# Kernel tuning notes

Hardware: AMD Instinct MI355X
Metric: run time of the kernel (lower is better)

The kernel has to match this reference:

```python
import jax, jax.numpy as jnp
import numpy as np

LEAKY_SLOPE = 0.01  # torch nn.LeakyReLU default

def leaky_relu(x):
    return jnp.where(x >= 0, x, LEAKY_SLOPE * x)

def setup_inputs() -> dict:
    key = jax.random.key(0)
    ks = jax.random.split(key, 11)
    B, F, C_IN, H, K, D = 2048, 512, 3, 64, 8, 128  # batch, features, expand, layer_conf[0], bucket_num, bucket_dim
    ASR, MM, OUT = 128, 768, 256
    proj_in = ASR + MM + F * D
    inp = {
        "stat_features": jax.random.uniform(ks[0], (B, F), dtype=jnp.float32),
        "asr_embeddings": jax.random.normal(ks[1], (B, ASR), dtype=jnp.float32),
        "mm_embeddings": jax.random.normal(ks[2], (B, MM), dtype=jnp.float32),
        "linear1_w": jax.random.normal(ks[3], (F, C_IN, H), dtype=jnp.float32) * (1.0 / np.sqrt(C_IN)),
        "linear1_b": jax.random.normal(ks[4], (F, 1, H), dtype=jnp.float32),
        "linear2_w": jax.random.normal(ks[5], (F, H, K), dtype=jnp.float32) * (1.0 / np.sqrt(H)),
        "linear2_b": jax.random.normal(ks[6], (F, 1, K), dtype=jnp.float32),
        "tau": jnp.ones((F, 1, K), dtype=jnp.float32),
        "emb": jax.random.normal(ks[7], (F, K, D), dtype=jnp.float32),
        "proj_w": jax.random.normal(ks[8], (OUT, proj_in), dtype=jnp.float32) * (1.0 / np.sqrt(proj_in)),
        "proj_b": jax.random.normal(ks[9], (OUT,), dtype=jnp.float32) * 0.01,
    }
    return inp

def reference(stat_features, asr_embeddings, mm_embeddings,
              linear1_w, linear1_b, linear2_w, linear2_b, tau, emb,
              proj_w, proj_b):
    # sanitize: NaN -> 0, negatives -> 0
    x = stat_features
    x = jnp.where(jnp.isnan(x) | (x < 0.0), 0.0, x)  # [B, F]

    # auto_dis: per-feature tiny MLP. x is expanded to 3 identical copies -> [B,F,1,3]
    # matmul with [F,3,H] == einsum over the 3 copies.
    B, F = x.shape
    x3 = jnp.broadcast_to(x[:, :, None], (B, F, 3))           # [B,F,3]
    h = jnp.einsum('bfc,fch->bfh', x3, linear1_w) + linear1_b[:, 0, :]  # [B,F,H]
    h = jnp.where(h >= 0, h, LEAKY_SLOPE * h)
    s = jnp.einsum('bfh,fhk->bfk', h, linear2_w) + linear2_b[:, 0, :]   # [B,F,K]
    s = jnp.where(s >= 0, s, LEAKY_SLOPE * s)
    s = s * tau[:, 0, :]
    p = jax.nn.softmax(s, axis=-1)                            # [B,F,K]
    y = jnp.einsum('bfk,fkd->bfd', p, emb)                    # [B,F,D]
    y = y.reshape(B, -1)                                      # [B, F*D] (fc = Identity)

    z = jnp.concatenate([asr_embeddings, mm_embeddings, y], axis=1)
    out = jax.nn.relu(z @ proj_w.T + proj_b)                  # [B, 256]
    return out
```

## Files before the change

### kernel.cpp

```cpp
#include <hip/hip_runtime.h>
#include <hip/hip_bf16.h>
#include <math.h>

#define LEAKY 0.01f
#define B_    2048
#define F_    512
#define H_    64
#define K_    8
#define D_    128
#define ASR_  128
#define MM_   768
#define OUT_  256
#define PROJ_IN 66432
#define ZK    4992
#define NSPLIT 8


typedef unsigned short u16;
typedef u16   u16x4 __attribute__((ext_vector_type(4)));
typedef u16   u16x8 __attribute__((ext_vector_type(8)));
typedef short s16x8 __attribute__((ext_vector_type(8)));
typedef float f32x4 __attribute__((ext_vector_type(4)));

__device__ __forceinline__ u16 f2bf(float x) {
  unsigned int u = __float_as_uint(x);
  u += 0x7fffu + ((u >> 16) & 1u);
  return (u16)(u >> 16);
}

#define PRODUCER_BLOCKS (2048 + 512 + 896 + 224)

__global__ __launch_bounds__(256) void producer_kernel(
    const float* __restrict__ stat, const float* __restrict__ w1,
    const float* __restrict__ b1v, const float* __restrict__ w2,
    const float* __restrict__ b2v, const float* __restrict__ tauv,
    const float* __restrict__ pw, const float* __restrict__ emb,
    const float* __restrict__ asr, const float* __restrict__ mm,
    u16* __restrict__ A0, u16* __restrict__ Pf, u16* __restrict__ Wn) {
  __shared__ __align__(16) char smem[20992];
  const int bid = blockIdx.x;
  const int t = threadIdx.x;

  if (bid < 2048) {
    const int f = bid >> 2;
    const int o0 = (bid & 3) * 64;
    float* s_emb = (float*)smem;
    for (int i = t; i < K_ * D_; i += 256) s_emb[i] = emb[(size_t)f * K_ * D_ + i];
    __syncthreads();
    const int orow = t >> 2, dc = t & 3;
    const float* src = pw + (size_t)(o0 + orow) * PROJ_IN + 896 + f * D_;
    float g[K_] = {0.f, 0.f, 0.f, 0.f, 0.f, 0.f, 0.f, 0.f};
    #pragma unroll
    for (int j = 0; j < 8; ++j) {
      const int d = dc * 4 + j * 16;
      float4 w = *(const float4*)(src + d);
      #pragma unroll
      for (int k = 0; k < K_; ++k) {
        float4 e = *(const float4*)(s_emb + k * D_ + d);
        g[k] = fmaf(w.x, e.x, g[k]);
        g[k] = fmaf(w.y, e.y, g[k]);
        g[k] = fmaf(w.z, e.z, g[k]);
        g[k] = fmaf(w.w, e.w, g[k]);
      }
    }
    #pragma unroll
    for (int k = 0; k < K_; ++k) {
      g[k] += __shfl_xor(g[k], 1);
      g[k] += __shfl_xor(g[k], 2);
    }
    if (dc == 0) {
      u16x8 hv;
      #pragma unroll
      for (int k = 0; k < K_; ++k) hv[k] = f2bf(g[k]);
      *(u16x8*)(Wn + (size_t)(o0 + orow) * ZK + 896 + f * K_) = hv;
    }
  } else if (bid < 2560) {
    const int pb = bid - 2048;
    const int f0 = (pb & 127) * 4;
    const int b0 = (pb >> 7) * 512;
    float* s_w1s = (float*)(smem);
    float* s_b1  = (float*)(smem + 1024);
    float* s_w2  = (float*)(smem + 2048);
    float* s_b2  = (float*)(smem + 10240);
    float* s_tau = (float*)(smem + 10368);
    float* s_x   = (float*)(smem + 10496);
    {
      int fl = t >> 6, h = t & 63;
      const float* wf = w1 + (size_t)(f0 + fl) * 192;
      s_w1s[fl * 64 + h] = wf[h] + wf[64 + h] + wf[128 + h];
      s_b1[fl * 64 + h] = b1v[(size_t)(f0 + fl) * 64 + h];
    }
    for (int i = t; i < 4 * 512; i += 256) {
      int fl = i >> 9, idx = i & 511;
      s_w2[fl * 512 + idx] = w2[(size_t)(f0 + fl) * 512 + idx];
    }
    if (t < 32) {
      s_b2[t]  = b2v[f0 * 8 + t];
      s_tau[t] = tauv[f0 * 8 + t];
    }
    for (int p = 0; p < 8; ++p) {
      int i = p * 256 + t;
      int r = i >> 2, fl = i & 3;
      float v = stat[(size_t)(b0 + r) * F_ + f0 + fl];
      s_x[r * 5 + fl] = (v >= 0.f) ? v : 0.f;
    }
    __syncthreads();

    const int w = t >> 6;
    const int lane = t & 63;
    const float* w1p = s_w1s + w * 64;
    const float* b1p = s_b1 + w * 64;
    const float* w2p = s_w2 + w * 512;
    float x[8];
    #pragma unroll
    for (int p = 0; p < 8; ++p) x[p] = s_x[(lane + 64 * p) * 5 + w];
    float acc[8][8] = {{0.f}};
    #pragma unroll 4
    for (int i = 0; i < 64; ++i) {
      float wv = w1p[i], bv = b1p[i];
      float4 wa = *(const float4*)(w2p + i * 8);
      float4 wb = *(const float4*)(w2p + i * 8 + 4);
      #pragma unroll
      for (int p = 0; p < 8; ++p) {
        float h0 = fmaf(x[p], wv, bv);
        float h = fmaf(LEAKY, fminf(h0, 0.f), fmaxf(h0, 0.f));
        acc[p][0] = fmaf(h, wa.x, acc[p][0]);
        acc[p][1] = fmaf(h, wa.y, acc[p][1]);
        acc[p][2] = fmaf(h, wa.z, acc[p][2]);
        acc[p][3] = fmaf(h, wa.w, acc[p][3]);
        acc[p][4] = fmaf(h, wb.x, acc[p][4]);
        acc[p][5] = fmaf(h, wb.y, acc[p][5]);
        acc[p][6] = fmaf(h, wb.z, acc[p][6]);
        acc[p][7] = fmaf(h, wb.w, acc[p][7]);
      }
    }
    #pragma unroll
    for (int p = 0; p < 8; ++p) {
      float s[K_];
      float m = -1e30f;
      #pragma unroll
      for (int k = 0; k < K_; ++k) {
        float v = acc[p][k] + s_b2[w * 8 + k];
        v = (v >= 0.f) ? v : LEAKY * v;
        v *= s_tau[w * 8 + k];
        s[k] = v;
        m = fmaxf(m, v);
      }
      float sum = 0.f;
      #pragma unroll
      for (int k = 0; k < K_; ++k) { s[k] = __expf(s[k] - m); sum += s[k]; }
      float inv = 1.f / sum;
      u16x8 hv;
      #pragma unroll
      for (int k = 0; k < K_; ++k) hv[k] = f2bf(s[k] * inv);
      *(u16x8*)(Pf + ((size_t)(f0 + w) * B_ + b0 + lane + 64 * p) * 8) = hv;
    }
  } else if (bid < 3456) {
    const int item = bid - 2560;
    const int cidx = item * 256 + t;
    const int r = cidx / 112, c = cidx % 112;
    float4 v0, v1;
    if (c < 16) {
      const float* s = asr + (size_t)r * ASR_ + c * 8;
      v0 = *(const float4*)(s); v1 = *(const float4*)(s + 4);
    } else {
      const float* s = mm + (size_t)r * MM_ + (c - 16) * 8;
      v0 = *(const float4*)(s); v1 = *(const float4*)(s + 4);
    }
    u16x8 hv = {f2bf(v0.x), f2bf(v0.y), f2bf(v0.z), f2bf(v0.w),
                f2bf(v1.x), f2bf(v1.y), f2bf(v1.z), f2bf(v1.w)};
    *(u16x8*)(A0 + (size_t)r * 896 + c * 8) = hv;
  } else {
    const int item = bid - 3456;
    #pragma unroll
    for (int rr = 0; rr < 4; ++rr) {
      int idx = item * 1024 + rr * 256 + t;
      int o = idx / 896, j = idx % 896;
      Wn[(size_t)o * ZK + j] = f2bf(pw[(size_t)o * PROJ_IN + j]);
    }
  }
}

#define SAS 72
__global__ __launch_bounds__(256) void gemm_kernel(
    const u16* __restrict__ A0, const u16* __restrict__ Pf,
    const u16* __restrict__ Wn, float* __restrict__ part) {
  const int bm0 = blockIdx.x * 64;
  const int bn0 = blockIdx.y * 64;
  const int kz  = blockIdx.z;
  const int it0 = kz * 10;
  const int itn = (kz == 7) ? 8 : 10;
  __shared__ u16 sA[64 * SAS];
  __shared__ u16 sB[64 * SAS];
  const int t = threadIdx.x;
  const int w = t >> 6, L = t & 63;
  const int l16 = L & 15, q8 = (L >> 4) * 8;
  const int wm = (w >> 1) * 32, wn = (w & 1) * 32;
  const int row = t >> 2, lk = t & 3;
  f32x4 acc[2][2] = {{{0.f,0.f,0.f,0.f},{0.f,0.f,0.f,0.f}},
                     {{0.f,0.f,0.f,0.f},{0.f,0.f,0.f,0.f}}};
  u16x8 ra[2], rb[2];

#define LOAD_TILES(IT)                                                        \
  {                                                                           \
    const int k0_ = (IT) * 64;                                                \
    if (k0_ < 896) {                                                          \
      const u16* s_ = A0 + (size_t)(bm0 + row) * 896 + k0_ + lk * 8;          \
      ra[0] = *(const u16x8*)(s_);                                            \
      ra[1] = *(const u16x8*)(s_ + 32);                                       \
    } else {                                                                  \
      const int fb_ = (k0_ - 896) >> 3;                                       \
      ra[0] = *(const u16x8*)(Pf + ((size_t)(fb_ + lk) * B_ + bm0 + row) * 8);\
      ra[1] = *(const u16x8*)(Pf + ((size_t)(fb_ + 4 + lk) * B_ + bm0 + row) * 8);\
    }                                                                         \
    const u16* sb_ = Wn + (size_t)(bn0 + row) * ZK + k0_ + lk * 8;            \
    rb[0] = *(const u16x8*)(sb_);                                             \
    rb[1] = *(const u16x8*)(sb_ + 32);                                        \
  }

#define STORE_TILES()                                                         \
  {                                                                           \
    *(u16x8*)&sA[row * SAS + lk * 8]      = ra[0];                            \
    *(u16x8*)&sA[row * SAS + lk * 8 + 32] = ra[1];                            \
    *(u16x8*)&sB[row * SAS + lk * 8]      = rb[0];                            \
    *(u16x8*)&sB[row * SAS + lk * 8 + 32] = rb[1];                            \
  }

  LOAD_TILES(it0);
  for (int it = it0; it < it0 + itn; ++it) {
    __syncthreads();
    STORE_TILES();
    __syncthreads();
    if (it + 1 < it0 + itn) LOAD_TILES(it + 1);
    #pragma unroll
    for (int ks = 0; ks < 2; ++ks) {
      s16x8 a0 = *(const s16x8*)&sA[(wm + l16) * SAS + ks * 32 + q8];
      s16x8 a1 = *(const s16x8*)&sA[(wm + 16 + l16) * SAS + ks * 32 + q8];
      s16x8 b0 = *(const s16x8*)&sB[(wn + l16) * SAS + ks * 32 + q8];
      s16x8 b1 = *(const s16x8*)&sB[(wn + 16 + l16) * SAS + ks * 32 + q8];
      acc[0][0] = __builtin_amdgcn_mfma_f32_16x16x32_bf16(a0, b0, acc[0][0], 0, 0, 0);
      acc[0][1] = __builtin_amdgcn_mfma_f32_16x16x32_bf16(a0, b1, acc[0][1], 0, 0, 0);
      acc[1][0] = __builtin_amdgcn_mfma_f32_16x16x32_bf16(a1, b0, acc[1][0], 0, 0, 0);
      acc[1][1] = __builtin_amdgcn_mfma_f32_16x16x32_bf16(a1, b1, acc[1][1], 0, 0, 0);
    }
  }
#undef LOAD_TILES
#undef STORE_TILES

  float* dst = part + (size_t)kz * B_ * OUT_;
  #pragma unroll
  for (int mf = 0; mf < 2; ++mf) {
    const int r0 = bm0 + wm + mf * 16 + (L >> 4) * 4;
    #pragma unroll
    for (int nf = 0; nf < 2; ++nf) {
      const int col = bn0 + wn + nf * 16 + l16;
      #pragma unroll
      for (int i = 0; i < 4; ++i)
        dst[(size_t)(r0 + i) * OUT_ + col] = acc[mf][nf][i];
    }
  }
}

__global__ __launch_bounds__(256) void combine_kernel(
    const float* __restrict__ part, const float* __restrict__ pb,
    float* __restrict__ out) {
  const int idx4 = (blockIdx.x * 256 + threadIdx.x) * 4;
  const int o = idx4 & (OUT_ - 1);
  float4 bv = *(const float4*)(pb + o);
  float4 r = bv;
  #pragma unroll
  for (int kz = 0; kz < NSPLIT; ++kz) {
    float4 a = *(const float4*)(part + (size_t)kz * B_ * OUT_ + idx4);
    r.x += a.x; r.y += a.y; r.z += a.z; r.w += a.w;
  }
  r.x = r.x > 0.f ? r.x : 0.f;
  r.y = r.y > 0.f ? r.y : 0.f;
  r.z = r.z > 0.f ? r.z : 0.f;
  r.w = r.w > 0.f ? r.w : 0.f;
  *(float4*)(out + idx4) = r;
}

extern "C" void kernel_launch(void* const* d_in, const int* in_sizes, int n_in,
                              void* d_out, int out_size, void* d_ws, size_t ws_size,
                              hipStream_t stream) {
  (void)in_sizes; (void)n_in; (void)out_size; (void)ws_size;
  const float* stat = (const float*)d_in[0];
  const float* asr  = (const float*)d_in[1];
  const float* mm   = (const float*)d_in[2];
  const float* w1   = (const float*)d_in[3];
  const float* b1   = (const float*)d_in[4];
  const float* w2   = (const float*)d_in[5];
  const float* b2   = (const float*)d_in[6];
  const float* tau  = (const float*)d_in[7];
  const float* emb  = (const float*)d_in[8];
  const float* pw   = (const float*)d_in[9];
  const float* pb   = (const float*)d_in[10];
  float* out = (float*)d_out;
  char* ws = (char*)d_ws;
  u16*   A0   = (u16*)(ws);
  u16*   Pf   = (u16*)(ws + 3670016);
  u16*   Wn   = (u16*)(ws + 20447232);
  float* part = (float*)(ws + 23003136);

  producer_kernel<<<PRODUCER_BLOCKS, 256, 0, stream>>>(
      stat, w1, b1, w2, b2, tau, pw, emb, asr, mm, A0, Pf, Wn);
  gemm_kernel<<<dim3(B_ / 64, OUT_ / 64, NSPLIT), 256, 0, stream>>>(
      A0, Pf, Wn, part);
  combine_kernel<<<B_ * OUT_ / 1024, 256, 0, stream>>>(part, pb, out);
}
```

Measured before the change: 172.8 us.

## Restructure emb-projection fold, halve softmax block batch, coalesce Pf gemm loads

The emb-folding section now handles 8 features by 32 output rows per block. It keeps emb in registers and streams proj_w rows through double-buffered shared memory with coalesced loads, replacing per-feature blocks that re-read proj_w with strided float4 loads. The auto_dis blocks process 256 batch rows instead of 512, doubling their count and halving register accumulators for better occupancy. The gemm's Pf tile load is remapped so consecutive threads read contiguous 16-byte chunks, with a matching transposed shared-memory store, at the cost of a per-iteration branch.

Result: faster. 161.7 us (-6.4%).

```diff
diff --git a/kernel.cpp b/kernel.cpp
--- a/kernel.cpp
+++ b/kernel.cpp
@@ -17,7 +17,6 @@
 
 
 typedef unsigned short u16;
-typedef u16   u16x4 __attribute__((ext_vector_type(4)));
 typedef u16   u16x8 __attribute__((ext_vector_type(8)));
 typedef short s16x8 __attribute__((ext_vector_type(8)));
 typedef float f32x4 __attribute__((ext_vector_type(4)));
@@ -28,7 +27,8 @@
   return (u16)(u >> 16);
 }
 
-#define PRODUCER_BLOCKS (2048 + 512 + 896 + 224)
+#define PRODUCER_BLOCKS (512 + 1024 + 896 + 224)
+#define PWS 132
 
 __global__ __launch_bounds__(256) void producer_kernel(
     const float* __restrict__ stat, const float* __restrict__ w1,
@@ -37,47 +37,48 @@
     const float* __restrict__ pw, const float* __restrict__ emb,
     const float* __restrict__ asr, const float* __restrict__ mm,
     u16* __restrict__ A0, u16* __restrict__ Pf, u16* __restrict__ Wn) {
-  __shared__ __align__(16) char smem[20992];
+  __shared__ __align__(16) char smem[15616];
   const int bid = blockIdx.x;
   const int t = threadIdx.x;
 
-  if (bid < 2048) {
-    const int f = bid >> 2;
-    const int o0 = (bid & 3) * 64;
-    float* s_emb = (float*)smem;
-    for (int i = t; i < K_ * D_; i += 256) s_emb[i] = emb[(size_t)f * K_ * D_ + i];
-    __syncthreads();
-    const int orow = t >> 2, dc = t & 3;
-    const float* src = pw + (size_t)(o0 + orow) * PROJ_IN + 896 + f * D_;
-    float g[K_] = {0.f, 0.f, 0.f, 0.f, 0.f, 0.f, 0.f, 0.f};
-    #pragma unroll
-    for (int j = 0; j < 8; ++j) {
-      const int d = dc * 4 + j * 16;
-      float4 w = *(const float4*)(src + d);
-      #pragma unroll
-      for (int k = 0; k < K_; ++k) {
-        float4 e = *(const float4*)(s_emb + k * D_ + d);
-        g[k] = fmaf(w.x, e.x, g[k]);
-        g[k] = fmaf(w.y, e.y, g[k]);
-        g[k] = fmaf(w.z, e.z, g[k]);
-        g[k] = fmaf(w.w, e.w, g[k]);
+  if (bid < 512) {
+    const int f0 = (bid >> 3) * 8;
+    const int o0 = (bid & 7) * 32;
+    float* s_pw = (float*)smem;
+    const int fl = t >> 5, k = (t >> 2) & 7, dq = t & 3;
+    float4 e[8];
+    {
+      const float* ep = emb + ((size_t)(f0 + fl) * 8 + k) * 128 + dq * 32;
+      #pragma unroll
+      for (int j = 0; j < 8; ++j) e[j] = *(const float4*)(ep + j * 4);
+    }
+    const int cf = t >> 5, cd = (t & 31) * 4;
+    const float* pwbase = pw + 896 + (size_t)f0 * 128 + (size_t)(o0)*PROJ_IN + t * 4;
+    float4 nxt = *(const float4*)(pwbase);
+    for (int r = 0; r < 32; ++r) {
+      float* buf = s_pw + (r & 1) * (8 * PWS);
+      *(float4*)(buf + cf * PWS + cd) = nxt;
+      __syncthreads();
+      if (r + 1 < 32) nxt = *(const float4*)(pwbase + (size_t)(r + 1) * PROJ_IN);
+      const float* pp = buf + fl * PWS + dq * 32;
+      float g = 0.f;
+      #pragma unroll
+      for (int j = 0; j < 8; ++j) {
+        float4 p4 = *(const float4*)(pp + j * 4);
+        g = fmaf(e[j].x, p4.x, g);
+        g = fmaf(e[j].y, p4.y, g);
+        g = fmaf(e[j].z, p4.z, g);
+        g = fmaf(e[j].w, p4.w, g);
       }
-    }
-    #pragma unroll
-    for (int k = 0; k < K_; ++k) {
-      g[k] += __shfl_xor(g[k], 1);
-      g[k] += __shfl_xor(g[k], 2);
-    }
-    if (dc == 0) {
-      u16x8 hv;
-      #pragma unroll
-      for (int k = 0; k < K_; ++k) hv[k] = f2bf(g[k]);
-      *(u16x8*)(Wn + (size_t)(o0 + orow) * ZK + 896 + f * K_) = hv;
-    }
-  } else if (bid < 2560) {
-    const int pb = bid - 2048;
+      g += __shfl_xor(g, 1);
+      g += __shfl_xor(g, 2);
+      if (dq == 0)
+        Wn[(size_t)(o0 + r) * ZK + 896 + (f0 + fl) * 8 + k] = f2bf(g);
+    }
+  } else if (bid < 1536) {
+    const int pb = bid - 512;
     const int f0 = (pb & 127) * 4;
-    const int b0 = (pb >> 7) * 512;
+    const int b0 = (pb >> 7) * 256;
     float* s_w1s = (float*)(smem);
     float* s_b1  = (float*)(smem + 1024);
     float* s_w2  = (float*)(smem + 2048);
@@ -98,7 +99,7 @@
       s_b2[t]  = b2v[f0 * 8 + t];
       s_tau[t] = tauv[f0 * 8 + t];
     }
-    for (int p = 0; p < 8; ++p) {
+    for (int p = 0; p < 4; ++p) {
       int i = p * 256 + t;
       int r = i >> 2, fl = i & 3;
       float v = stat[(size_t)(b0 + r) * F_ + f0 + fl];
@@ -111,17 +112,17 @@
     const float* w1p = s_w1s + w * 64;
     const float* b1p = s_b1 + w * 64;
     const float* w2p = s_w2 + w * 512;
-    float x[8];
-    #pragma unroll
-    for (int p = 0; p < 8; ++p) x[p] = s_x[(lane + 64 * p) * 5 + w];
-    float acc[8][8] = {{0.f}};
+    float x[4];
+    #pragma unroll
+    for (int p = 0; p < 4; ++p) x[p] = s_x[(lane + 64 * p) * 5 + w];
+    float acc[4][8] = {{0.f}};
     #pragma unroll 4
     for (int i = 0; i < 64; ++i) {
       float wv = w1p[i], bv = b1p[i];
       float4 wa = *(const float4*)(w2p + i * 8);
       float4 wb = *(const float4*)(w2p + i * 8 + 4);
       #pragma unroll
-      for (int p = 0; p < 8; ++p) {
+      for (int p = 0; p < 4; ++p) {
         float h0 = fmaf(x[p], wv, bv);
         float h = fmaf(LEAKY, fminf(h0, 0.f), fmaxf(h0, 0.f));
         acc[p][0] = fmaf(h, wa.x, acc[p][0]);
@@ -135,28 +136,28 @@
       }
     }
     #pragma unroll
-    for (int p = 0; p < 8; ++p) {
+    for (int p = 0; p < 4; ++p) {
       float s[K_];
       float m = -1e30f;
       #pragma unroll
-      for (int k = 0; k < K_; ++k) {
-        float v = acc[p][k] + s_b2[w * 8 + k];
+      for (int kk = 0; kk < K_; ++kk) {
+        float v = acc[p][kk] + s_b2[w * 8 + kk];
         v = (v >= 0.f) ? v : LEAKY * v;
-        v *= s_tau[w * 8 + k];
-        s[k] = v;
+        v *= s_tau[w * 8 + kk];
+        s[kk] = v;
         m = fmaxf(m, v);
       }
       float sum = 0.f;
       #pragma unroll
-      for (int k = 0; k < K_; ++k) { s[k] = __expf(s[k] - m); sum += s[k]; }
+      for (int kk = 0; kk < K_; ++kk) { s[kk] = __expf(s[kk] - m); sum += s[kk]; }
       float inv = 1.f / sum;
       u16x8 hv;
       #pragma unroll
-      for (int k = 0; k < K_; ++k) hv[k] = f2bf(s[k] * inv);
+      for (int kk = 0; kk < K_; ++kk) hv[kk] = f2bf(s[kk] * inv);
       *(u16x8*)(Pf + ((size_t)(f0 + w) * B_ + b0 + lane + 64 * p) * 8) = hv;
     }
-  } else if (bid < 3456) {
-    const int item = bid - 2560;
+  } else if (bid < 2432) {
+    const int item = bid - 1536;
     const int cidx = item * 256 + t;
     const int r = cidx / 112, c = cidx % 112;
     float4 v0, v1;
@@ -171,7 +172,7 @@
                 f2bf(v1.x), f2bf(v1.y), f2bf(v1.z), f2bf(v1.w)};
     *(u16x8*)(A0 + (size_t)r * 896 + c * 8) = hv;
   } else {
-    const int item = bid - 3456;
+    const int item = bid - 2432;
     #pragma unroll
     for (int rr = 0; rr < 4; ++rr) {
       int idx = item * 1024 + rr * 256 + t;
@@ -197,6 +198,7 @@
   const int l16 = L & 15, q8 = (L >> 4) * 8;
   const int wm = (w >> 1) * 32, wn = (w & 1) * 32;
   const int row = t >> 2, lk = t & 3;
+  const int pp = t >> 5, pg = t & 31;
   f32x4 acc[2][2] = {{{0.f,0.f,0.f,0.f},{0.f,0.f,0.f,0.f}},
                      {{0.f,0.f,0.f,0.f},{0.f,0.f,0.f,0.f}}};
   u16x8 ra[2], rb[2];
@@ -210,18 +212,24 @@
       ra[1] = *(const u16x8*)(s_ + 32);                                       \
     } else {                                                                  \
       const int fb_ = (k0_ - 896) >> 3;                                       \
-      ra[0] = *(const u16x8*)(Pf + ((size_t)(fb_ + lk) * B_ + bm0 + row) * 8);\
-      ra[1] = *(const u16x8*)(Pf + ((size_t)(fb_ + 4 + lk) * B_ + bm0 + row) * 8);\
+      const u16* s_ = Pf + ((size_t)(fb_ + pp) * B_ + bm0 + pg) * 8;          \
+      ra[0] = *(const u16x8*)(s_);                                            \
+      ra[1] = *(const u16x8*)(s_ + 256);                        \
     }                                                                         \
     const u16* sb_ = Wn + (size_t)(bn0 + row) * ZK + k0_ + lk * 8;            \
     rb[0] = *(const u16x8*)(sb_);                                             \
     rb[1] = *(const u16x8*)(sb_ + 32);                                        \
   }
 
-#define STORE_TILES()                                                         \
+#define STORE_TILES(IT)                                                       \
   {                                                                           \
-    *(u16x8*)&sA[row * SAS + lk * 8]      = ra[0];                            \
-    *(u16x8*)&sA[row * SAS + lk * 8 + 32] = ra[1];                            \
+    if ((IT) * 64 < 896) {                                                    \
+      *(u16x8*)&sA[row * SAS + lk * 8]      = ra[0];                          \
+      *(u16x8*)&sA[row * SAS + lk * 8 + 32] = ra[1];                          \
+    } else {                                                                  \
+      *(u16x8*)&sA[pg * SAS + pp * 8]        = ra[0];                         \
+      *(u16x8*)&sA[(pg + 32) * SAS + pp * 8] = ra[1];                         \
+    }                                                                         \
     *(u16x8*)&sB[row * SAS + lk * 8]      = rb[0];                            \
     *(u16x8*)&sB[row * SAS + lk * 8 + 32] = rb[1];                            \
   }
@@ -229,7 +237,7 @@
   LOAD_TILES(it0);
   for (int it = it0; it < it0 + itn; ++it) {
     __syncthreads();
-    STORE_TILES();
+    STORE_TILES(it);
     __syncthreads();
     if (it + 1 < it0 + itn) LOAD_TILES(it + 1);
     #pragma unroll
```
